# Kernel optimization log

Measured on AMD Instinct MI355X. Metric: run time of the kernel, lower is better.

The kernel has to match this reference:

```python
import jax, jax.numpy as jnp
import numpy as np

N_NODES = 50000
N_EDGES = 800000
IN, HID, OUT = 96, 96, 64


def setup_inputs() -> dict:
    key = jax.random.key(0)
    ks = jax.random.split(key, 12)
    x = jax.random.normal(ks[0], (N_NODES, IN), dtype=jnp.float32)
    src = jax.random.randint(ks[1], (N_EDGES,), 0, N_NODES, dtype=jnp.int32)
    dst = jax.random.randint(ks[2], (N_EDGES,), 0, N_NODES, dtype=jnp.int32)
    dims = [(IN, HID), (HID, HID), (HID, OUT)]
    params = {}
    for i, (din, dout) in enumerate(dims):
        s = 1.0 / np.sqrt(din)
        params[f"w_self{i}"] = jax.random.uniform(ks[3 + 3 * i], (dout, din), jnp.float32, -s, s)
        params[f"w_neigh{i}"] = jax.random.uniform(ks[4 + 3 * i], (dout, din), jnp.float32, -s, s)
        params[f"b{i}"] = jnp.zeros((dout,), jnp.float32)
    return {"x": x, "src": src, "dst": dst, **params}


def _sage_layer(h, src, dst, w_self, w_neigh, b):
    # mean aggregation of source-node features onto destination nodes
    msum = jax.ops.segment_sum(h[src], dst, num_segments=N_NODES)  # [N, d]
    deg = jax.ops.segment_sum(jnp.ones((src.shape[0],), h.dtype), dst, num_segments=N_NODES)
    hmean = msum / jnp.maximum(deg, 1.0)[:, None]
    return h @ w_self.T + hmean @ w_neigh.T + b


def reference(x, src, dst,
              w_self0, w_neigh0, b0,
              w_self1, w_neigh1, b1,
              w_self2, w_neigh2, b2):
    # Layer 0 + ReLU (dropout is identity in eval mode)
    h = jax.nn.relu(_sage_layer(x, src, dst, w_self0, w_neigh0, b0))
    # Layer 1 + ReLU
    h = jax.nn.relu(_sage_layer(h, src, dst, w_self1, w_neigh1, b1))
    # Final layer, no activation
    h = _sage_layer(h, src, dst, w_self2, w_neigh2, b2)
    return h
```

## Files before the change

kernel.cpp:

```cpp
#include <hip/hip_runtime.h>
#include <hip/hip_fp16.h>


#define DIN 96

typedef __attribute__((ext_vector_type(8))) short bf16x8;
typedef __attribute__((ext_vector_type(16))) float f32x16;

__global__ void zero_deg_kernel(int* __restrict__ p, int n) {
    int i = blockIdx.x * blockDim.x + threadIdx.x;
    if (i < n) p[i] = 0;
}

__global__ void deg_kernel(const int* __restrict__ dst, int* __restrict__ deg,
                           int* __restrict__ rank, int nE) {
    int i = blockIdx.x * blockDim.x + threadIdx.x;
    if (i < nE) rank[i] = atomicAdd(&deg[dst[i]], 1);
}

__global__ void block_sum_kernel(const int* __restrict__ deg, int* __restrict__ bsum, int nN) {
    __shared__ int s[256];
    const int tid = threadIdx.x;
    int i = blockIdx.x * 256 + tid;
    s[tid] = (i < nN) ? deg[i] : 0;
    __syncthreads();
    for (int d = 128; d > 0; d >>= 1) {
        if (tid < d) s[tid] += s[tid + d];
        __syncthreads();
    }
    if (tid == 0) bsum[blockIdx.x] = s[0];
}

__global__ void bsum_scan_kernel(int* __restrict__ bsum, int nB) {
    __shared__ int s[256];
    const int tid = threadIdx.x;
    int v = (tid < nB) ? bsum[tid] : 0;
    s[tid] = v;
    __syncthreads();
    for (int d = 1; d < 256; d <<= 1) {
        int t = (tid >= d) ? s[tid - d] : 0;
        __syncthreads();
        s[tid] += t;
        __syncthreads();
    }
    if (tid < nB) bsum[tid] = s[tid] - v;
}

__global__ void scan_apply_kernel(const int* __restrict__ deg, const int* __restrict__ bsum,
                                  int* __restrict__ offs, int nN) {
    __shared__ int s[256];
    const int tid = threadIdx.x;
    int i = blockIdx.x * 256 + tid;
    int v = (i < nN) ? deg[i] : 0;
    s[tid] = v;
    __syncthreads();
    for (int d = 1; d < 256; d <<= 1) {
        int t = (tid >= d) ? s[tid - d] : 0;
        __syncthreads();
        s[tid] += t;
        __syncthreads();
    }
    if (i < nN) offs[i] = bsum[blockIdx.x] + s[tid] - v;
}

__global__ void bucket_kernel(const int* __restrict__ src, const int* __restrict__ dst,
                              const int* __restrict__ offs, const int* __restrict__ rank,
                              unsigned short* __restrict__ esrc, int nE) {
    int e = blockIdx.x * blockDim.x + threadIdx.x;
    if (e < nE) esrc[offs[dst[e]] + rank[e]] = (unsigned short)src[e];
}

__global__ void tof16_kernel(const float* __restrict__ x, __half* __restrict__ xf, int n8) {
    int i = blockIdx.x * blockDim.x + threadIdx.x;
    if (i >= n8) return;
    float4 f0 = *reinterpret_cast<const float4*>(x + (size_t)i * 8);
    float4 f1 = *reinterpret_cast<const float4*>(x + (size_t)i * 8 + 4);
    union { __half2 h2[4]; float4 raw; } o;
    o.h2[0] = __float22half2_rn(make_float2(f0.x, f0.y));
    o.h2[1] = __float22half2_rn(make_float2(f0.z, f0.w));
    o.h2[2] = __float22half2_rn(make_float2(f1.x, f1.y));
    o.h2[3] = __float22half2_rn(make_float2(f1.z, f1.w));
    *reinterpret_cast<float4*>(xf + (size_t)i * 8) = o.raw;
}

__global__ void gather_kernel(const __half* __restrict__ hf, const unsigned short* __restrict__ esrc,
                              const int* __restrict__ offs, const int* __restrict__ deg,
                              __half* __restrict__ hmean, int nN) {
    int idx = blockIdx.x * blockDim.x + threadIdx.x;
    if (idx >= nN * 12) return;
    int n = idx / 12;
    int q = idx - n * 12;
    const int beg = offs[n];
    const int dg = deg[n];
    const int end = beg + dg;
    const __half* hq = hf + q * 8;

    union H8 { float4 raw; __half2 h2[4]; };
    float a0[8], a1[8], a2[8], a3[8];
#pragma unroll
    for (int k = 0; k < 8; ++k) { a0[k] = 0.f; a1[k] = 0.f; a2[k] = 0.f; a3[k] = 0.f; }

    int j = beg;
    for (; j + 4 <= end; j += 4) {
        int s0 = esrc[j], s1 = esrc[j + 1], s2 = esrc[j + 2], s3 = esrc[j + 3];
        H8 v0, v1, v2, v3;
        v0.raw = *reinterpret_cast<const float4*>(hq + (size_t)s0 * DIN);
        v1.raw = *reinterpret_cast<const float4*>(hq + (size_t)s1 * DIN);
        v2.raw = *reinterpret_cast<const float4*>(hq + (size_t)s2 * DIN);
        v3.raw = *reinterpret_cast<const float4*>(hq + (size_t)s3 * DIN);
#pragma unroll
        for (int k = 0; k < 4; ++k) {
            float2 f0 = __half22float2(v0.h2[k]);
            float2 f1 = __half22float2(v1.h2[k]);
            float2 f2 = __half22float2(v2.h2[k]);
            float2 f3 = __half22float2(v3.h2[k]);
            a0[2 * k] += f0.x; a0[2 * k + 1] += f0.y;
            a1[2 * k] += f1.x; a1[2 * k + 1] += f1.y;
            a2[2 * k] += f2.x; a2[2 * k + 1] += f2.y;
            a3[2 * k] += f3.x; a3[2 * k + 1] += f3.y;
        }
    }
    for (; j < end; ++j) {
        int s0 = esrc[j];
        H8 v0;
        v0.raw = *reinterpret_cast<const float4*>(hq + (size_t)s0 * DIN);
#pragma unroll
        for (int k = 0; k < 4; ++k) {
            float2 f0 = __half22float2(v0.h2[k]);
            a0[2 * k] += f0.x; a0[2 * k + 1] += f0.y;
        }
    }
    const float r = 1.0f / (float)max(dg, 1);
    union H8 o;
    o.h2[0] = __float22half2_rn(make_float2((a0[0]+a1[0]+a2[0]+a3[0])*r, (a0[1]+a1[1]+a2[1]+a3[1])*r));
    o.h2[1] = __float22half2_rn(make_float2((a0[2]+a1[2]+a2[2]+a3[2])*r, (a0[3]+a1[3]+a2[3]+a3[3])*r));
    o.h2[2] = __float22half2_rn(make_float2((a0[4]+a1[4]+a2[4]+a3[4])*r, (a0[5]+a1[5]+a2[5]+a3[5])*r));
    o.h2[3] = __float22half2_rn(make_float2((a0[6]+a1[6]+a2[6]+a3[6])*r, (a0[7]+a1[7]+a2[7]+a3[7])*r));
    *reinterpret_cast<float4*>(hmean + (size_t)n * DIN + q * 8) = o.raw;
}

__device__ __forceinline__ void fv8_to_hilo(const float* fv, bf16x8& hi, bf16x8& lo) {
    union { unsigned int u[4]; bf16x8 v; } H, L;
#pragma unroll
    for (int i = 0; i < 4; ++i) {
        unsigned u0 = __float_as_uint(fv[2 * i]);
        unsigned u1 = __float_as_uint(fv[2 * i + 1]);
        unsigned h0 = u0 & 0xFFFF0000u;
        unsigned h1 = u1 & 0xFFFF0000u;
        H.u[i] = h1 | (h0 >> 16);
        float l0 = fv[2 * i]     - __uint_as_float(h0);
        float l1 = fv[2 * i + 1] - __uint_as_float(h1);
        L.u[i] = (__float_as_uint(l1) & 0xFFFF0000u) | (__float_as_uint(l0) >> 16);
    }
    hi = H.v; lo = L.v;
}

template<int DOUT, int NP, bool RELU, bool FINAL>
__global__ __launch_bounds__(256)
void sage_gemm_mfma(const __half* __restrict__ hp, const __half* __restrict__ hm,
                    const float* __restrict__ wself, const float* __restrict__ wneigh,
                    const float* __restrict__ bias, float* __restrict__ fout,
                    __half* __restrict__ hout, int nN) {
    __shared__ unsigned int WhiS[DOUT][100];
    __shared__ unsigned int WloS[DOUT][100];

    const int tid = threadIdx.x;
    const int n0 = blockIdx.x * 256;

    for (int c = tid; c < DOUT * 24; c += 256) {
        int r = c / 24, k8 = c - (c / 24) * 24;
        const float* srcw = (k8 < 12) ? (wself + (size_t)r * 96 + k8 * 8)
                                      : (wneigh + (size_t)r * 96 + (k8 - 12) * 8);
        float4 f0 = *reinterpret_cast<const float4*>(srcw);
        float4 f1 = *reinterpret_cast<const float4*>(srcw + 4);
        float fv[8] = {f0.x, f0.y, f0.z, f0.w, f1.x, f1.y, f1.z, f1.w};
        bf16x8 hi, lo;
        fv8_to_hilo(fv, hi, lo);
        *reinterpret_cast<bf16x8*>(&WhiS[r][k8 * 4]) = hi;
        *reinterpret_cast<bf16x8*>(&WloS[r][k8 * 4]) = lo;
    }
    __syncthreads();

    const int lane = tid & 63;
    const int w = tid >> 6;
    const int col = lane & 31;
    const int q = lane >> 5;
    const int mbase = n0 + w * 64;

    const int nA0 = min(mbase + col, nN - 1);
    const int nA1 = min(mbase + 32 + col, nN - 1);

    f32x16 acc[NP][2];
#pragma unroll
    for (int p = 0; p < NP; ++p) {
        f32x16 z = {};
        acc[p][0] = z;
        acc[p][1] = z;
    }

#pragma unroll
    for (int ks = 0; ks < 12; ++ks) {
        const __half* s0 = (ks < 6) ? (hp + (size_t)nA0 * 96 + ks * 16 + q * 8)
                                    : (hm + (size_t)nA0 * 96 + (ks - 6) * 16 + q * 8);
        const __half* s1 = (ks < 6) ? (hp + (size_t)nA1 * 96 + ks * 16 + q * 8)
                                    : (hm + (size_t)nA1 * 96 + (ks - 6) * 16 + q * 8);
        union { float4 raw; __half2 h2[4]; } u0, u1;
        u0.raw = *reinterpret_cast<const float4*>(s0);
        u1.raw = *reinterpret_cast<const float4*>(s1);
        float fv0[8], fv1[8];
#pragma unroll
        for (int k = 0; k < 4; ++k) {
            float2 f0 = __half22float2(u0.h2[k]);
            float2 f1 = __half22float2(u1.h2[k]);
            fv0[2 * k] = f0.x; fv0[2 * k + 1] = f0.y;
            fv1[2 * k] = f1.x; fv1[2 * k + 1] = f1.y;
        }
        bf16x8 ahi0, alo0, ahi1, alo1;
        fv8_to_hilo(fv0, ahi0, alo0);
        fv8_to_hilo(fv1, ahi1, alo1);

#pragma unroll
        for (int p = 0; p < NP; ++p) {
            const bf16x8 whi = *reinterpret_cast<const bf16x8*>(&WhiS[p * 32 + col][ks * 8 + q * 4]);
            const bf16x8 wlo = *reinterpret_cast<const bf16x8*>(&WloS[p * 32 + col][ks * 8 + q * 4]);
            acc[p][0] = __builtin_amdgcn_mfma_f32_32x32x16_bf16(ahi0, whi, acc[p][0], 0, 0, 0);
            acc[p][0] = __builtin_amdgcn_mfma_f32_32x32x16_bf16(ahi0, wlo, acc[p][0], 0, 0, 0);
            acc[p][0] = __builtin_amdgcn_mfma_f32_32x32x16_bf16(alo0, whi, acc[p][0], 0, 0, 0);
            acc[p][1] = __builtin_amdgcn_mfma_f32_32x32x16_bf16(ahi1, whi, acc[p][1], 0, 0, 0);
            acc[p][1] = __builtin_amdgcn_mfma_f32_32x32x16_bf16(ahi1, wlo, acc[p][1], 0, 0, 0);
            acc[p][1] = __builtin_amdgcn_mfma_f32_32x32x16_bf16(alo1, whi, acc[p][1], 0, 0, 0);
        }
    }

#pragma unroll
    for (int p = 0; p < NP; ++p) {
        const int oc = p * 32 + col;
        const float bv = bias[oc];
#pragma unroll
        for (int i = 0; i < 16; ++i) {
            const int row = (i & 3) + 8 * (i >> 2) + 4 * q;
            int n = mbase + row;
            if (n < nN) {
                float v = acc[p][0][i] + bv;
                if (RELU) v = fmaxf(v, 0.f);
                if (FINAL) fout[(size_t)n * DOUT + oc] = v;
                else       hout[(size_t)n * DOUT + oc] = __float2half_rn(v);
            }
            n = mbase + 32 + row;
            if (n < nN) {
                float v = acc[p][1][i] + bv;
                if (RELU) v = fmaxf(v, 0.f);
                if (FINAL) fout[(size_t)n * DOUT + oc] = v;
                else       hout[(size_t)n * DOUT + oc] = __float2half_rn(v);
            }
        }
    }
}

extern "C" void kernel_launch(void* const* d_in, const int* in_sizes, int n_in,
                              void* d_out, int out_size, void* d_ws, size_t ws_size,
                              hipStream_t stream) {
    const float* x   = (const float*)d_in[0];
    const int*   src = (const int*)d_in[1];
    const int*   dst = (const int*)d_in[2];
    const float* ws0 = (const float*)d_in[3];
    const float* wn0 = (const float*)d_in[4];
    const float* b0  = (const float*)d_in[5];
    const float* ws1 = (const float*)d_in[6];
    const float* wn1 = (const float*)d_in[7];
    const float* b1  = (const float*)d_in[8];
    const float* ws2 = (const float*)d_in[9];
    const float* wn2 = (const float*)d_in[10];
    const float* b2  = (const float*)d_in[11];
    float* out = (float*)d_out;

    const int nN = in_sizes[0] / DIN;
    const int nE = in_sizes[1];
    const int nB = (nN + 255) / 256;

    int* deg  = (int*)d_ws;
    int* offs = deg + 50048;
    int* bsum = offs + 50048;
    int* rank = bsum + 256;
    unsigned short* esrc = (unsigned short*)(rank + nE);
    __half* hp16 = (__half*)(esrc + nE);
    __half* hm16 = hp16 + (size_t)nN * DIN;

    zero_deg_kernel<<<nB, 256, 0, stream>>>(deg, nN);
    deg_kernel<<<(nE + 255) / 256, 256, 0, stream>>>(dst, deg, rank, nE);
    block_sum_kernel<<<nB, 256, 0, stream>>>(deg, bsum, nN);
    bsum_scan_kernel<<<1, 256, 0, stream>>>(bsum, nB);
    scan_apply_kernel<<<nB, 256, 0, stream>>>(deg, bsum, offs, nN);
    bucket_kernel<<<(nE + 255) / 256, 256, 0, stream>>>(src, dst, offs, rank, esrc, nE);

    const int cgrid = (nN * 12 + 255) / 256;
    const int ggrid = (nN * 12 + 255) / 256;
    const int mgrid = (nN + 255) / 256;

    tof16_kernel<<<cgrid, 256, 0, stream>>>(x, hp16, nN * 12);
    gather_kernel<<<ggrid, 256, 0, stream>>>(hp16, esrc, offs, deg, hm16, nN);
    sage_gemm_mfma<96, 3, true, false><<<mgrid, 256, 0, stream>>>(hp16, hm16, ws0, wn0, b0, nullptr, hp16, nN);

    gather_kernel<<<ggrid, 256, 0, stream>>>(hp16, esrc, offs, deg, hm16, nN);
    sage_gemm_mfma<96, 3, true, false><<<mgrid, 256, 0, stream>>>(hp16, hm16, ws1, wn1, b1, nullptr, hp16, nN);

    gather_kernel<<<ggrid, 256, 0, stream>>>(hp16, esrc, offs, deg, hm16, nN);
    sage_gemm_mfma<64, 2, false, true><<<mgrid, 256, 0, stream>>>(hp16, hm16, ws2, wn2, b2, out, nullptr, nN);
}
```

Before: 217.6 us.

## Fuse CSR build and fp16 conversion into one cooperative kernel with grid syncs

Replaces the six preprocessing kernels and the fp16 conversion kernel with a single cooperative kernel of 1024 blocks. Grid-wide syncs separate the phases: conversion plus degree zeroing, atomic degree counting, block sums, the bsum scan, offset apply and bucketing. This removes several launch gaps and tail drains. In exchange it adds grid.sync costs, and the scan phases assume nN/256 (196) fits within the 1024 blocks. Cooperative launch also requires that all 1024 blocks be co-resident.

```diff
diff --git a/kernel.cpp b/kernel.cpp
--- a/kernel.cpp
+++ b/kernel.cpp
@@ -1,5 +1,8 @@
 #include <hip/hip_runtime.h>
 #include <hip/hip_fp16.h>
+#include <hip/hip_cooperative_groups.h>
+
+namespace cg = cooperative_groups;
 
 
 #define DIN 96
@@ -7,80 +10,78 @@
 typedef __attribute__((ext_vector_type(8))) short bf16x8;
 typedef __attribute__((ext_vector_type(16))) float f32x16;
 
-__global__ void zero_deg_kernel(int* __restrict__ p, int n) {
-    int i = blockIdx.x * blockDim.x + threadIdx.x;
-    if (i < n) p[i] = 0;
-}
-
-__global__ void deg_kernel(const int* __restrict__ dst, int* __restrict__ deg,
-                           int* __restrict__ rank, int nE) {
-    int i = blockIdx.x * blockDim.x + threadIdx.x;
-    if (i < nE) rank[i] = atomicAdd(&deg[dst[i]], 1);
-}
-
-__global__ void block_sum_kernel(const int* __restrict__ deg, int* __restrict__ bsum, int nN) {
+__global__ void __launch_bounds__(256)
+csr_build_kernel(const float* __restrict__ x, __half* __restrict__ hp16,
+                 const int* __restrict__ src, const int* __restrict__ dst,
+                 int* __restrict__ deg, int* __restrict__ offs,
+                 int* __restrict__ bsum, int* __restrict__ rank,
+                 unsigned short* __restrict__ esrc, int nN, int nE, int n8) {
+    cg::grid_group grid = cg::this_grid();
+    const int tid = threadIdx.x;
+    const int gid = blockIdx.x * 256 + tid;
+    const int gsz = gridDim.x * 256;
     __shared__ int s[256];
-    const int tid = threadIdx.x;
-    int i = blockIdx.x * 256 + tid;
-    s[tid] = (i < nN) ? deg[i] : 0;
-    __syncthreads();
-    for (int d = 128; d > 0; d >>= 1) {
-        if (tid < d) s[tid] += s[tid + d];
+
+    for (int i = gid; i < n8; i += gsz) {
+        float4 f0 = *reinterpret_cast<const float4*>(x + (size_t)i * 8);
+        float4 f1 = *reinterpret_cast<const float4*>(x + (size_t)i * 8 + 4);
+        union { __half2 h2[4]; float4 raw; } o;
+        o.h2[0] = __float22half2_rn(make_float2(f0.x, f0.y));
+        o.h2[1] = __float22half2_rn(make_float2(f0.z, f0.w));
+        o.h2[2] = __float22half2_rn(make_float2(f1.x, f1.y));
+        o.h2[3] = __float22half2_rn(make_float2(f1.z, f1.w));
+        *reinterpret_cast<float4*>(hp16 + (size_t)i * 8) = o.raw;
+    }
+    for (int i = gid; i < nN; i += gsz) deg[i] = 0;
+    grid.sync();
+
+    for (int e = gid; e < nE; e += gsz) rank[e] = atomicAdd(&deg[dst[e]], 1);
+    grid.sync();
+
+    const int nScanB = (nN + 255) / 256;
+    if (blockIdx.x < (unsigned)nScanB) {
+        int i = blockIdx.x * 256 + tid;
+        s[tid] = (i < nN) ? deg[i] : 0;
         __syncthreads();
-    }
-    if (tid == 0) bsum[blockIdx.x] = s[0];
-}
-
-__global__ void bsum_scan_kernel(int* __restrict__ bsum, int nB) {
-    __shared__ int s[256];
-    const int tid = threadIdx.x;
-    int v = (tid < nB) ? bsum[tid] : 0;
-    s[tid] = v;
-    __syncthreads();
-    for (int d = 1; d < 256; d <<= 1) {
-        int t = (tid >= d) ? s[tid - d] : 0;
+        for (int d = 128; d > 0; d >>= 1) {
+            if (tid < d) s[tid] += s[tid + d];
+            __syncthreads();
+        }
+        if (tid == 0) bsum[blockIdx.x] = s[0];
+    }
+    grid.sync();
+
+    if (blockIdx.x == 0) {
+        int v = (tid < nScanB) ? bsum[tid] : 0;
+        s[tid] = v;
         __syncthreads();
-        s[tid] += t;
+        for (int d = 1; d < 256; d <<= 1) {
+            int t = (tid >= d) ? s[tid - d] : 0;
+            __syncthreads();
+            s[tid] += t;
+            __syncthreads();
+        }
+        if (tid < nScanB) bsum[tid] = s[tid] - v;
+    }
+    grid.sync();
+
+    if (blockIdx.x < (unsigned)nScanB) {
+        int i = blockIdx.x * 256 + tid;
+        int v = (i < nN) ? deg[i] : 0;
+        s[tid] = v;
         __syncthreads();
-    }
-    if (tid < nB) bsum[tid] = s[tid] - v;
-}
-
-__global__ void scan_apply_kernel(const int* __restrict__ deg, const int* __restrict__ bsum,
-                                  int* __restrict__ offs, int nN) {
-    __shared__ int s[256];
-    const int tid = threadIdx.x;
-    int i = blockIdx.x * 256 + tid;
-    int v = (i < nN) ? deg[i] : 0;
-    s[tid] = v;
-    __syncthreads();
-    for (int d = 1; d < 256; d <<= 1) {
-        int t = (tid >= d) ? s[tid - d] : 0;
-        __syncthreads();
-        s[tid] += t;
-        __syncthreads();
-    }
-    if (i < nN) offs[i] = bsum[blockIdx.x] + s[tid] - v;
-}
-
-__global__ void bucket_kernel(const int* __restrict__ src, const int* __restrict__ dst,
-                              const int* __restrict__ offs, const int* __restrict__ rank,
-                              unsigned short* __restrict__ esrc, int nE) {
-    int e = blockIdx.x * blockDim.x + threadIdx.x;
-    if (e < nE) esrc[offs[dst[e]] + rank[e]] = (unsigned short)src[e];
-}
-
-__global__ void tof16_kernel(const float* __restrict__ x, __half* __restrict__ xf, int n8) {
-    int i = blockIdx.x * blockDim.x + threadIdx.x;
-    if (i >= n8) return;
-    float4 f0 = *reinterpret_cast<const float4*>(x + (size_t)i * 8);
-    float4 f1 = *reinterpret_cast<const float4*>(x + (size_t)i * 8 + 4);
-    union { __half2 h2[4]; float4 raw; } o;
-    o.h2[0] = __float22half2_rn(make_float2(f0.x, f0.y));
-    o.h2[1] = __float22half2_rn(make_float2(f0.z, f0.w));
-    o.h2[2] = __float22half2_rn(make_float2(f1.x, f1.y));
-    o.h2[3] = __float22half2_rn(make_float2(f1.z, f1.w));
-    *reinterpret_cast<float4*>(xf + (size_t)i * 8) = o.raw;
+        for (int d = 1; d < 256; d <<= 1) {
+            int t = (tid >= d) ? s[tid - d] : 0;
+            __syncthreads();
+            s[tid] += t;
+            __syncthreads();
+        }
+        if (i < nN) offs[i] = bsum[blockIdx.x] + s[tid] - v;
+    }
+    grid.sync();
+
+    for (int e = gid; e < nE; e += gsz)
+        esrc[offs[dst[e]] + rank[e]] = (unsigned short)src[e];
 }
 
 __global__ void gather_kernel(const __half* __restrict__ hf, const unsigned short* __restrict__ esrc,
@@ -274,9 +275,9 @@
     const float* b2  = (const float*)d_in[11];
     float* out = (float*)d_out;
 
-    const int nN = in_sizes[0] / DIN;
-    const int nE = in_sizes[1];
-    const int nB = (nN + 255) / 256;
+    int nN = in_sizes[0] / DIN;
+    int nE = in_sizes[1];
+    int n8 = nN * 12;
 
     int* deg  = (int*)d_ws;
     int* offs = deg + 50048;
@@ -286,18 +287,17 @@
     __half* hp16 = (__half*)(esrc + nE);
     __half* hm16 = hp16 + (size_t)nN * DIN;
 
-    zero_deg_kernel<<<nB, 256, 0, stream>>>(deg, nN);
-    deg_kernel<<<(nE + 255) / 256, 256, 0, stream>>>(dst, deg, rank, nE);
-    block_sum_kernel<<<nB, 256, 0, stream>>>(deg, bsum, nN);
-    bsum_scan_kernel<<<1, 256, 0, stream>>>(bsum, nB);
-    scan_apply_kernel<<<nB, 256, 0, stream>>>(deg, bsum, offs, nN);
-    bucket_kernel<<<(nE + 255) / 256, 256, 0, stream>>>(src, dst, offs, rank, esrc, nE);
-
-    const int cgrid = (nN * 12 + 255) / 256;
+    {
+        void* args[] = {(void*)&x, (void*)&hp16, (void*)&src, (void*)&dst,
+                        (void*)&deg, (void*)&offs, (void*)&bsum, (void*)&rank,
+                        (void*)&esrc, (void*)&nN, (void*)&nE, (void*)&n8};
+        hipLaunchCooperativeKernel((void*)csr_build_kernel, dim3(1024), dim3(256),
+                                   args, 0, stream);
+    }
+
     const int ggrid = (nN * 12 + 255) / 256;
     const int mgrid = (nN + 255) / 256;
 
-    tof16_kernel<<<cgrid, 256, 0, stream>>>(x, hp16, nN * 12);
     gather_kernel<<<ggrid, 256, 0, stream>>>(hp16, esrc, offs, deg, hm16, nN);
     sage_gemm_mfma<96, 3, true, false><<<mgrid, 256, 0, stream>>>(hp16, hm16, ws0, wn0, b0, nullptr, hp16, nN);
 
```

New measurement: 714.0 us. 3.28x slower.
